# Kernel optimization log

Hardware: AMD Instinct MI355X
Metric: run time of the kernel (lower is better)

## Reference

```python
import jax, jax.numpy as jnp
import numpy as np

N = 50000   # node_count
D = 64      # dim_in (also GCN hidden, GRU hidden, top-k k)
E = 800000  # num_edges


def setup_inputs() -> dict:
    key = jax.random.key(0)
    ks = jax.random.split(key, 10)
    s = 1.0 / np.sqrt(D)
    return {
        "x": jax.random.normal(ks[0], (N, D), jnp.float32),
        "edge_index": jax.random.randint(ks[1], (2, E), 0, N, dtype=jnp.int64),
        "edge_weight": jax.random.uniform(ks[2], (E,), jnp.float32),
        # TopKPooling projection vector p
        "pool_p": jax.random.normal(ks[3], (D,), jnp.float32) * s,
        # EvolveGCNH initial weight (GRU hidden state h0), [D, D]
        "init_W": jax.random.normal(ks[4], (D, D), jnp.float32) * s,
        # GRU params, torch gate order (r, z, n)
        "gru_Wih": jax.random.normal(ks[5], (3 * D, D), jnp.float32) * s,
        "gru_Whh": jax.random.normal(ks[6], (3 * D, D), jnp.float32) * s,
        "gru_bih": jax.random.normal(ks[7], (3 * D,), jnp.float32) * s,
        "gru_bhh": jax.random.normal(ks[8], (3 * D,), jnp.float32) * s,
        # final Linear(D, 1)
        "lin_W": jax.random.normal(ks[9], (1, D), jnp.float32) * s,
        "lin_b": jnp.zeros((1,), jnp.float32),
    }


def reference(x, edge_index, edge_weight, pool_p, init_W,
              gru_Wih, gru_Whh, gru_bih, gru_bhh, lin_W, lin_b):
    n, d = x.shape
    # ---- TopKPooling: k = ceil((D/N) * N) = D nodes ----
    score = (x @ pool_p) / jnp.linalg.norm(pool_p)          # [N]
    vals, perm = jax.lax.top_k(score, d)                    # descending, k = D
    x_tilde = x[perm] * jnp.tanh(vals)[:, None]             # [D, D]
    # ---- one GRU step: batch = D pooled nodes, hidden = D, h0 = init_W ----
    gi = x_tilde @ gru_Wih.T + gru_bih                      # [D, 3D]
    gh = init_W @ gru_Whh.T + gru_bhh                       # [D, 3D]
    i_r, i_z, i_n = jnp.split(gi, 3, axis=-1)
    h_r, h_z, h_n = jnp.split(gh, 3, axis=-1)
    r = jax.nn.sigmoid(i_r + h_r)
    z = jax.nn.sigmoid(i_z + h_z)
    nn_ = jnp.tanh(i_n + r * h_n)
    W = (1.0 - z) * nn_ + z * init_W                        # evolved GCN weight [D, D]
    # ---- GCNConv_Fixed_W: add self-loops + symmetric norm + scatter ----
    loop = jnp.arange(n)
    row = jnp.concatenate([edge_index[0], loop])            # sources
    col = jnp.concatenate([edge_index[1], loop])            # targets
    w = jnp.concatenate([edge_weight, jnp.ones((n,), x.dtype)])
    deg = jax.ops.segment_sum(w, col, num_segments=n)
    deg_safe = jnp.where(deg > 0, deg, 1.0)
    dinv = jnp.where(deg > 0, jax.lax.rsqrt(deg_safe), 0.0)
    norm = dinv[row] * w * dinv[col]                        # [E+N]
    xw = x @ W                                              # [N, D]
    agg = jax.ops.segment_sum(norm[:, None] * xw[row], col, num_segments=n)
    # ---- head: relu + Linear(D, 1) ----
    h = jax.nn.relu(agg)
    return h @ lin_W.T + lin_b                              # [N, 1]
```

## Files before the change

kernel.cpp:

```cpp
#include <hip/hip_runtime.h>
#include <hip/hip_fp16.h>
#include <cmath>

#define N_NODES 50000
#define DIM 64
#define E_EDGES 800000
#define SCAN_BLOCKS 196
#define FIX 16777216.0f
#define DEG_MASK 0xFFFFFFFFFFull
#define NB_A 98
#define NRUNS 98

__global__ __launch_bounds__(256) void init_kernel(
    unsigned long long* __restrict__ packed, int* __restrict__ fillc) {
    int g = blockIdx.x * blockDim.x + threadIdx.x;
    if (g < N_NODES) { packed[g] = 0ull; fillc[g] = 0; }
}

__device__ __forceinline__ void wave_sort64(float& v, int& idx, int lane) {
    #pragma unroll
    for (int k = 2; k <= 64; k <<= 1) {
        #pragma unroll
        for (int j = k >> 1; j > 0; j >>= 1) {
            float ov = __shfl_xor(v, j);
            int   oi = __shfl_xor(idx, j);
            bool lower = ((lane & j) == 0);
            bool up    = ((lane & k) == 0);
            bool mine_prec = (v > ov) || (v == ov && idx < oi);
            bool keep = up ? (lower == mine_prec) : (lower != mine_prec);
            if (!keep) { v = ov; idx = oi; }
        }
    }
}

__device__ __forceinline__ void wave_merge_top64(float& v, int& idx,
                                                 float bv, int bi, int lane) {
    bool a_prec = (v > bv) || (v == bv && idx < bi);
    if (!a_prec) { v = bv; idx = bi; }
    #pragma unroll
    for (int j = 32; j > 0; j >>= 1) {
        float ov = __shfl_xor(v, j);
        int   oi = __shfl_xor(idx, j);
        bool lower = ((lane & j) == 0);
        bool mine_prec = (v > ov) || (v == ov && idx < oi);
        bool keep = (lower == mine_prec);
        if (!keep) { v = ov; idx = oi; }
    }
}

__global__ __launch_bounds__(512) void score_topk_a_kernel(
    const float* __restrict__ x, const float* __restrict__ p,
    float* __restrict__ cand_val, int* __restrict__ cand_idx,
    const int* __restrict__ ei, const float* __restrict__ ew,
    unsigned long long* __restrict__ packed) {
    __shared__ float sv[512];
    __shared__ int   si[512];
    int t = threadIdx.x, lane = t & 63, wvid = t >> 6;
    int g = blockIdx.x * 512 + t;
    float v; int idx;
    if (g < N_NODES) {
        const float4* x4 = (const float4*)(x + (size_t)g * DIM);
        const float4* p4 = (const float4*)p;
        float dot = 0.f, pn = 0.f;
        #pragma unroll
        for (int k = 0; k < 16; k++) {
            float4 xv = x4[k], pv = p4[k];
            dot += xv.x * pv.x + xv.y * pv.y + xv.z * pv.z + xv.w * pv.w;
            pn  += pv.x * pv.x + pv.y * pv.y + pv.z * pv.z + pv.w * pv.w;
        }
        v = dot / sqrtf(pn);
        idx = g;
    } else { v = -INFINITY; idx = 0x7fffffff; }
    wave_sort64(v, idx, lane);
    sv[t] = v; si[t] = idx;
    __syncthreads();
    if (wvid == 0) {
        #pragma unroll
        for (int r = 1; r < 8; r++)
            wave_merge_top64(v, idx, sv[r * 64 + 63 - lane], si[r * 64 + 63 - lane], lane);
        cand_val[blockIdx.x * 64 + lane] = v;
        cand_idx[blockIdx.x * 64 + lane] = idx;
    }
    for (int e = blockIdx.x * 512 + t; e < E_EDGES; e += NB_A * 512) {
        int c = ei[E_EDGES + e];
        unsigned long long q = (unsigned long long)(ew[e] * FIX);
        atomicAdd(&packed[c], (1ull << 40) | q);
    }
}

__global__ __launch_bounds__(256) void scan1_kernel(
    const unsigned long long* __restrict__ packed,
    int* __restrict__ off, int* __restrict__ bsum, float* __restrict__ dinv) {
    __shared__ int s[256];
    int t = threadIdx.x;
    int g = blockIdx.x * 256 + t;
    unsigned long long pk = (g < N_NODES) ? packed[g] : 0ull;
    int v = (int)(pk >> 40);
    if (g < N_NODES)
        dinv[g] = rsqrtf((float)(pk & DEG_MASK) * (1.0f / FIX) + 1.0f);
    s[t] = v;
    __syncthreads();
    for (int d = 1; d < 256; d <<= 1) {
        int add = (t >= d) ? s[t - d] : 0;
        __syncthreads();
        s[t] += add;
        __syncthreads();
    }
    if (g < N_NODES) off[g] = s[t] - v;
    if (t == 255) bsum[blockIdx.x] = s[255];
}

__global__ __launch_bounds__(256) void scan2_kernel(
    const int* __restrict__ bsum, int* __restrict__ boff) {
    __shared__ int s[256];
    int t = threadIdx.x;
    int v = (t < SCAN_BLOCKS) ? bsum[t] : 0;
    s[t] = v;
    __syncthreads();
    for (int d = 1; d < 256; d <<= 1) {
        int add = (t >= d) ? s[t - d] : 0;
        __syncthreads();
        s[t] += add;
        __syncthreads();
    }
    boff[t] = s[t] - v;
}

__global__ __launch_bounds__(256) void fill_kernel(
    const int* __restrict__ ei, const float* __restrict__ ew,
    const float* __restrict__ dinv, const int* __restrict__ off,
    const int* __restrict__ boff, int* __restrict__ fillc,
    float2* __restrict__ ren) {
    int e = blockIdx.x * blockDim.x + threadIdx.x;
    if (e >= E_EDGES) return;
    int r = ei[e], c = ei[E_EDGES + e];
    int pos = off[c] + boff[c >> 8] + atomicAdd(&fillc[c], 1);
    ren[pos] = make_float2(__int_as_float(r), dinv[r] * ew[e] * dinv[c]);
}

__global__ __launch_bounds__(1024) void topk_b_kernel(
    const float* __restrict__ cand_val, const int* __restrict__ cand_idx,
    const float* __restrict__ x, float* __restrict__ x_tilde) {
    __shared__ float rsv[16 * 64];
    __shared__ int   rsi[16 * 64];
    __shared__ float tval[64];
    __shared__ int   perm[64];
    int t = threadIdx.x, lane = t & 63, wv = t >> 6;
    int r0 = wv * 8;
    float v; int idx;
    if (r0 < NRUNS) { v = cand_val[r0 * 64 + lane]; idx = cand_idx[r0 * 64 + lane]; }
    else            { v = -INFINITY; idx = 0x7fffffff; }
    for (int r = r0 + 1; r < r0 + 8 && r < NRUNS; r++)
        wave_merge_top64(v, idx, cand_val[r * 64 + 63 - lane],
                         cand_idx[r * 64 + 63 - lane], lane);
    rsv[wv * 64 + lane] = v; rsi[wv * 64 + lane] = idx;
    __syncthreads();
    if (wv == 0) {
        v = rsv[lane]; idx = rsi[lane];
        for (int r = 1; r < 16; r++)
            wave_merge_top64(v, idx, rsv[r * 64 + 63 - lane],
                             rsi[r * 64 + 63 - lane], lane);
        tval[lane] = tanhf(v);
        perm[lane] = idx;
    }
    __syncthreads();
    for (int i = t; i < 4096; i += 1024) {
        int j = i >> 6, kk = i & 63;
        x_tilde[i] = x[perm[j] * DIM + kk] * tval[j];
    }
}

__global__ __launch_bounds__(64) void gru_kernel(
    const float* __restrict__ xt, const float* __restrict__ initW,
    const float* __restrict__ Wih, const float* __restrict__ Whh,
    const float* __restrict__ bih, const float* __restrict__ bhh,
    float* __restrict__ Wout) {
    __shared__ float xrow[64], hrow[64];
    int i = blockIdx.x, j = threadIdx.x;
    xrow[j] = xt[i * 64 + j];
    hrow[j] = initW[i * 64 + j];
    __syncthreads();
    float gi_r = bih[j], gi_z = bih[j + 64], gi_n = bih[j + 128];
    float gh_r = bhh[j], gh_z = bhh[j + 64], gh_n = bhh[j + 128];
    for (int k = 0; k < 64; k++) {
        float xv = xrow[k], hv = hrow[k];
        gi_r += xv * Wih[j * 64 + k];
        gi_z += xv * Wih[(j + 64) * 64 + k];
        gi_n += xv * Wih[(j + 128) * 64 + k];
        gh_r += hv * Whh[j * 64 + k];
        gh_z += hv * Whh[(j + 64) * 64 + k];
        gh_n += hv * Whh[(j + 128) * 64 + k];
    }
    float r = 1.f / (1.f + expf(-(gi_r + gh_r)));
    float z = 1.f / (1.f + expf(-(gi_z + gh_z)));
    float nn = tanhf(gi_n + r * gh_n);
    Wout[i * 64 + j] = (1.f - z) * nn + z * hrow[j];
}

__global__ __launch_bounds__(256) void xw_kernel(
    const float* __restrict__ x, const float* __restrict__ W,
    __half* __restrict__ xwh) {
    __shared__ float Wl[64 * 64];
    __shared__ float Xl[64 * 64];
    int t = threadIdx.x;
    int r0 = blockIdx.x * 64;
    for (int i = t; i < 4096; i += 256) Wl[i] = W[i];
    for (int i = t; i < 4096; i += 256) {
        int r = r0 + (i >> 6);
        Xl[i] = (r < N_NODES) ? x[r0 * 64 + i] : 0.f;
    }
    __syncthreads();
    int j = t & 63, ty = t >> 6;
    float acc[16];
    #pragma unroll
    for (int rr = 0; rr < 16; rr++) acc[rr] = 0.f;
    for (int k = 0; k < 64; k++) {
        float wvv = Wl[k * 64 + j];
        #pragma unroll
        for (int rr = 0; rr < 16; rr++)
            acc[rr] += Xl[(ty * 16 + rr) * 64 + k] * wvv;
    }
    #pragma unroll
    for (int rr = 0; rr < 16; rr++) {
        int r = r0 + ty * 16 + rr;
        if (r < N_NODES) xwh[r * DIM + j] = __float2half(acc[rr]);
    }
}

__global__ __launch_bounds__(256) void gather_head_kernel(
    const int* __restrict__ off, const int* __restrict__ boff,
    const float2* __restrict__ ren, const float* __restrict__ dinv,
    const float4* __restrict__ xwh,
    const float* __restrict__ linW, const float* __restrict__ linb,
    float* __restrict__ out) {
    int gid = blockIdx.x * blockDim.x + threadIdx.x;
    int n = gid >> 6, lane = gid & 63;
    if (n >= N_NODES) return;
    int c8 = lane & 7;
    int slot = lane >> 3;
    float acc[8];
    #pragma unroll
    for (int q = 0; q < 8; q++) acc[q] = 0.f;
    if (slot == 0) {
        float di = dinv[n];
        float s = di * di;
        float4 hv = xwh[n * 8 + c8];
        const __half2* h2 = reinterpret_cast<const __half2*>(&hv);
        #pragma unroll
        for (int q = 0; q < 4; q++) {
            float2 f = __half22float2(h2[q]);
            acc[2 * q]     = s * f.x;
            acc[2 * q + 1] = s * f.y;
        }
    }
    int s0 = off[n] + boff[n >> 8];
    int e0 = (n == N_NODES - 1) ? E_EDGES : off[n + 1] + boff[(n + 1) >> 8];
    for (int base = s0; base < e0; base += 64) {
        int m = min(64, e0 - base);
        int rv = 0; float wv = 0.f;
        if (base + lane < e0) {
            float2 pk = ren[base + lane];
            rv = __float_as_int(pk.x);
            wv = pk.y;
        }
        int G = (m + 7) >> 3;
        int g = 0;
        for (; g + 2 <= G; g += 2) {
            int src0 = g * 8 + slot, src1 = src0 + 8;
            int   ra = __shfl(rv, src0);  float wa = __shfl(wv, src0);
            int   rb = __shfl(rv, src1);  float wb = __shfl(wv, src1);
            float4 ha = xwh[ra * 8 + c8];
            float4 hb = xwh[rb * 8 + c8];
            const __half2* h2a = reinterpret_cast<const __half2*>(&ha);
            const __half2* h2b = reinterpret_cast<const __half2*>(&hb);
            #pragma unroll
            for (int q = 0; q < 4; q++) {
                float2 fa = __half22float2(h2a[q]);
                float2 fb = __half22float2(h2b[q]);
                acc[2 * q]     += wa * fa.x + wb * fb.x;
                acc[2 * q + 1] += wa * fa.y + wb * fb.y;
            }
        }
        if (g < G) {
            int src = g * 8 + slot;
            int r = __shfl(rv, src);
            float ww = __shfl(wv, src);
            float4 hv = xwh[r * 8 + c8];
            const __half2* h2 = reinterpret_cast<const __half2*>(&hv);
            #pragma unroll
            for (int q = 0; q < 4; q++) {
                float2 f = __half22float2(h2[q]);
                acc[2 * q]     += ww * f.x;
                acc[2 * q + 1] += ww * f.y;
            }
        }
    }
    #pragma unroll
    for (int q = 0; q < 8; q++) {
        acc[q] += __shfl_xor(acc[q], 8);
        acc[q] += __shfl_xor(acc[q], 16);
        acc[q] += __shfl_xor(acc[q], 32);
    }
    float pv = 0.f;
    #pragma unroll
    for (int q = 0; q < 8; q++)
        pv += fmaxf(acc[q], 0.f) * linW[c8 * 8 + q];
    pv += __shfl_xor(pv, 1); pv += __shfl_xor(pv, 2); pv += __shfl_xor(pv, 4);
    if (lane == 0) out[n] = pv + linb[0];
}

extern "C" void kernel_launch(void* const* d_in, const int* in_sizes, int n_in,
                              void* d_out, int out_size, void* d_ws, size_t ws_size,
                              hipStream_t stream) {
    const float* x     = (const float*)d_in[0];
    const int*   ei    = (const int*)d_in[1];
    const float* ew    = (const float*)d_in[2];
    const float* p     = (const float*)d_in[3];
    const float* initW = (const float*)d_in[4];
    const float* Wih   = (const float*)d_in[5];
    const float* Whh   = (const float*)d_in[6];
    const float* bih   = (const float*)d_in[7];
    const float* bhh   = (const float*)d_in[8];
    const float* linW  = (const float*)d_in[9];
    const float* linb  = (const float*)d_in[10];
    float* out = (float*)d_out;

    char* w = (char*)d_ws;
    unsigned long long* packed = (unsigned long long*)w; w += 8ull * N_NODES;
    int*   fillc   = (int*)w;      w += 4ull * N_NODES;
    float2* ren    = (float2*)w;   w += 8ull * E_EDGES;
    __half* xwh    = (__half*)w;   w += 2ull * (size_t)N_NODES * DIM;
    float* dinv    = (float*)w;    w += 4ull * N_NODES;
    int*   off     = (int*)w;      w += 4ull * N_NODES;
    float* cand_val= (float*)w;    w += 4ull * 8192;
    int*   cand_idx= (int*)w;      w += 4ull * 8192;
    float* x_tilde = (float*)w;    w += 4ull * 4096;
    float* W       = (float*)w;    w += 4ull * 4096;
    int*   bsum    = (int*)w;      w += 4ull * 256;
    int*   boff    = (int*)w;      w += 4ull * 256;

    init_kernel<<<SCAN_BLOCKS, 256, 0, stream>>>(packed, fillc);
    score_topk_a_kernel<<<NB_A, 512, 0, stream>>>(x, p, cand_val, cand_idx, ei, ew, packed);
    topk_b_kernel<<<1, 1024, 0, stream>>>(cand_val, cand_idx, x, x_tilde);
    gru_kernel<<<64, 64, 0, stream>>>(x_tilde, initW, Wih, Whh, bih, bhh, W);
    xw_kernel<<<(N_NODES + 63) / 64, 256, 0, stream>>>(x, W, xwh);
    scan1_kernel<<<SCAN_BLOCKS, 256, 0, stream>>>(packed, off, bsum, dinv);
    scan2_kernel<<<1, 256, 0, stream>>>(bsum, boff);
    fill_kernel<<<(E_EDGES + 255) / 256, 256, 0, stream>>>(ei, ew, dinv, off, boff, fillc, ren);
    gather_head_kernel<<<(N_NODES * 64 + 255) / 256, 256, 0, stream>>>(
        off, boff, ren, dinv, (const float4*)xwh, linW, linb, out);
}
```

Measured before the change: 247.8 us.

## Fuse topk-B with scan1 and GRU with scan2, widen edge-degree atomics grid

Merges the single-block top-k merge with the degree scan (extra blocks handle 1024-node scan chunks) and merges the GRU step with the second-level scan, cutting two kernel launches from the serial chain. The edge-degree atomic loop now runs over 384 blocks instead of 98, with only the first 98 doing scoring, to spread the atomic traffic. The scan block size grows from 256 to 1024, so boff indexing changes to >>10. This trades launch overhead for a longer serial 1024-thread scan and uneven block work inside the fused kernels.

```diff
diff --git a/kernel.cpp b/kernel.cpp
--- a/kernel.cpp
+++ b/kernel.cpp
@@ -5,11 +5,12 @@
 #define N_NODES 50000
 #define DIM 64
 #define E_EDGES 800000
-#define SCAN_BLOCKS 196
 #define FIX 16777216.0f
 #define DEG_MASK 0xFFFFFFFFFFull
 #define NB_A 98
+#define NB_EDGE 384
 #define NRUNS 98
+#define SCAN1_BLOCKS 49
 
 __global__ __launch_bounds__(256) void init_kernel(
     unsigned long long* __restrict__ packed, int* __restrict__ fillc) {
@@ -56,134 +57,127 @@
     __shared__ float sv[512];
     __shared__ int   si[512];
     int t = threadIdx.x, lane = t & 63, wvid = t >> 6;
-    int g = blockIdx.x * 512 + t;
-    float v; int idx;
-    if (g < N_NODES) {
-        const float4* x4 = (const float4*)(x + (size_t)g * DIM);
-        const float4* p4 = (const float4*)p;
-        float dot = 0.f, pn = 0.f;
-        #pragma unroll
-        for (int k = 0; k < 16; k++) {
-            float4 xv = x4[k], pv = p4[k];
-            dot += xv.x * pv.x + xv.y * pv.y + xv.z * pv.z + xv.w * pv.w;
-            pn  += pv.x * pv.x + pv.y * pv.y + pv.z * pv.z + pv.w * pv.w;
-        }
-        v = dot / sqrtf(pn);
-        idx = g;
-    } else { v = -INFINITY; idx = 0x7fffffff; }
-    wave_sort64(v, idx, lane);
-    sv[t] = v; si[t] = idx;
-    __syncthreads();
-    if (wvid == 0) {
-        #pragma unroll
-        for (int r = 1; r < 8; r++)
-            wave_merge_top64(v, idx, sv[r * 64 + 63 - lane], si[r * 64 + 63 - lane], lane);
-        cand_val[blockIdx.x * 64 + lane] = v;
-        cand_idx[blockIdx.x * 64 + lane] = idx;
-    }
-    for (int e = blockIdx.x * 512 + t; e < E_EDGES; e += NB_A * 512) {
+    if (blockIdx.x < NB_A) {
+        int g = blockIdx.x * 512 + t;
+        float v; int idx;
+        if (g < N_NODES) {
+            const float4* x4 = (const float4*)(x + (size_t)g * DIM);
+            const float4* p4 = (const float4*)p;
+            float dot = 0.f, pn = 0.f;
+            #pragma unroll
+            for (int k = 0; k < 16; k++) {
+                float4 xv = x4[k], pv = p4[k];
+                dot += xv.x * pv.x + xv.y * pv.y + xv.z * pv.z + xv.w * pv.w;
+                pn  += pv.x * pv.x + pv.y * pv.y + pv.z * pv.z + pv.w * pv.w;
+            }
+            v = dot / sqrtf(pn);
+            idx = g;
+        } else { v = -INFINITY; idx = 0x7fffffff; }
+        wave_sort64(v, idx, lane);
+        sv[t] = v; si[t] = idx;
+        __syncthreads();
+        if (wvid == 0) {
+            #pragma unroll
+            for (int r = 1; r < 8; r++)
+                wave_merge_top64(v, idx, sv[r * 64 + 63 - lane], si[r * 64 + 63 - lane], lane);
+            cand_val[blockIdx.x * 64 + lane] = v;
+            cand_idx[blockIdx.x * 64 + lane] = idx;
+        }
+    }
+    for (int e = blockIdx.x * 512 + t; e < E_EDGES; e += NB_EDGE * 512) {
         int c = ei[E_EDGES + e];
         unsigned long long q = (unsigned long long)(ew[e] * FIX);
         atomicAdd(&packed[c], (1ull << 40) | q);
     }
 }
 
-__global__ __launch_bounds__(256) void scan1_kernel(
+__global__ __launch_bounds__(1024) void topkb_scan1_kernel(
+    const float* __restrict__ cand_val, const int* __restrict__ cand_idx,
+    const float* __restrict__ x, float* __restrict__ x_tilde,
     const unsigned long long* __restrict__ packed,
     int* __restrict__ off, int* __restrict__ bsum, float* __restrict__ dinv) {
-    __shared__ int s[256];
-    int t = threadIdx.x;
-    int g = blockIdx.x * 256 + t;
-    unsigned long long pk = (g < N_NODES) ? packed[g] : 0ull;
-    int v = (int)(pk >> 40);
-    if (g < N_NODES)
-        dinv[g] = rsqrtf((float)(pk & DEG_MASK) * (1.0f / FIX) + 1.0f);
-    s[t] = v;
-    __syncthreads();
-    for (int d = 1; d < 256; d <<= 1) {
-        int add = (t >= d) ? s[t - d] : 0;
-        __syncthreads();
-        s[t] += add;
-        __syncthreads();
-    }
-    if (g < N_NODES) off[g] = s[t] - v;
-    if (t == 255) bsum[blockIdx.x] = s[255];
-}
-
-__global__ __launch_bounds__(256) void scan2_kernel(
-    const int* __restrict__ bsum, int* __restrict__ boff) {
-    __shared__ int s[256];
-    int t = threadIdx.x;
-    int v = (t < SCAN_BLOCKS) ? bsum[t] : 0;
-    s[t] = v;
-    __syncthreads();
-    for (int d = 1; d < 256; d <<= 1) {
-        int add = (t >= d) ? s[t - d] : 0;
-        __syncthreads();
-        s[t] += add;
-        __syncthreads();
-    }
-    boff[t] = s[t] - v;
-}
-
-__global__ __launch_bounds__(256) void fill_kernel(
-    const int* __restrict__ ei, const float* __restrict__ ew,
-    const float* __restrict__ dinv, const int* __restrict__ off,
-    const int* __restrict__ boff, int* __restrict__ fillc,
-    float2* __restrict__ ren) {
-    int e = blockIdx.x * blockDim.x + threadIdx.x;
-    if (e >= E_EDGES) return;
-    int r = ei[e], c = ei[E_EDGES + e];
-    int pos = off[c] + boff[c >> 8] + atomicAdd(&fillc[c], 1);
-    ren[pos] = make_float2(__int_as_float(r), dinv[r] * ew[e] * dinv[c]);
-}
-
-__global__ __launch_bounds__(1024) void topk_b_kernel(
-    const float* __restrict__ cand_val, const int* __restrict__ cand_idx,
-    const float* __restrict__ x, float* __restrict__ x_tilde) {
     __shared__ float rsv[16 * 64];
     __shared__ int   rsi[16 * 64];
     __shared__ float tval[64];
     __shared__ int   perm[64];
+    __shared__ int   s_scan[1024];
     int t = threadIdx.x, lane = t & 63, wv = t >> 6;
-    int r0 = wv * 8;
-    float v; int idx;
-    if (r0 < NRUNS) { v = cand_val[r0 * 64 + lane]; idx = cand_idx[r0 * 64 + lane]; }
-    else            { v = -INFINITY; idx = 0x7fffffff; }
-    for (int r = r0 + 1; r < r0 + 8 && r < NRUNS; r++)
-        wave_merge_top64(v, idx, cand_val[r * 64 + 63 - lane],
-                         cand_idx[r * 64 + 63 - lane], lane);
-    rsv[wv * 64 + lane] = v; rsi[wv * 64 + lane] = idx;
-    __syncthreads();
-    if (wv == 0) {
-        v = rsv[lane]; idx = rsi[lane];
-        for (int r = 1; r < 16; r++)
-            wave_merge_top64(v, idx, rsv[r * 64 + 63 - lane],
-                             rsi[r * 64 + 63 - lane], lane);
-        tval[lane] = tanhf(v);
-        perm[lane] = idx;
-    }
-    __syncthreads();
-    for (int i = t; i < 4096; i += 1024) {
-        int j = i >> 6, kk = i & 63;
-        x_tilde[i] = x[perm[j] * DIM + kk] * tval[j];
-    }
-}
-
-__global__ __launch_bounds__(64) void gru_kernel(
+    if (blockIdx.x == 0) {
+        int r0 = wv * 8;
+        float v; int idx;
+        if (r0 < NRUNS) { v = cand_val[r0 * 64 + lane]; idx = cand_idx[r0 * 64 + lane]; }
+        else            { v = -INFINITY; idx = 0x7fffffff; }
+        for (int r = r0 + 1; r < r0 + 8 && r < NRUNS; r++)
+            wave_merge_top64(v, idx, cand_val[r * 64 + 63 - lane],
+                             cand_idx[r * 64 + 63 - lane], lane);
+        rsv[wv * 64 + lane] = v; rsi[wv * 64 + lane] = idx;
+        __syncthreads();
+        if (wv == 0) {
+            v = rsv[lane]; idx = rsi[lane];
+            for (int r = 1; r < 16; r++)
+                wave_merge_top64(v, idx, rsv[r * 64 + 63 - lane],
+                                 rsi[r * 64 + 63 - lane], lane);
+            tval[lane] = tanhf(v);
+            perm[lane] = idx;
+        }
+        __syncthreads();
+        for (int i = t; i < 4096; i += 1024) {
+            int j = i >> 6, kk = i & 63;
+            x_tilde[i] = x[perm[j] * DIM + kk] * tval[j];
+        }
+    } else {
+        int b = blockIdx.x - 1;
+        int g = b * 1024 + t;
+        unsigned long long pk = (g < N_NODES) ? packed[g] : 0ull;
+        int v = (int)(pk >> 40);
+        if (g < N_NODES)
+            dinv[g] = rsqrtf((float)(pk & DEG_MASK) * (1.0f / FIX) + 1.0f);
+        s_scan[t] = v;
+        __syncthreads();
+        for (int d = 1; d < 1024; d <<= 1) {
+            int add = (t >= d) ? s_scan[t - d] : 0;
+            __syncthreads();
+            s_scan[t] += add;
+            __syncthreads();
+        }
+        if (g < N_NODES) off[g] = s_scan[t] - v;
+        if (t == 1023) bsum[b] = s_scan[1023];
+    }
+}
+
+__global__ __launch_bounds__(256) void gru_scan2_kernel(
+    const int* __restrict__ bsum, int* __restrict__ boff,
     const float* __restrict__ xt, const float* __restrict__ initW,
     const float* __restrict__ Wih, const float* __restrict__ Whh,
     const float* __restrict__ bih, const float* __restrict__ bhh,
     float* __restrict__ Wout) {
-    __shared__ float xrow[64], hrow[64];
-    int i = blockIdx.x, j = threadIdx.x;
-    xrow[j] = xt[i * 64 + j];
-    hrow[j] = initW[i * 64 + j];
+    __shared__ float xrow_s[256], hrow_s[256];
+    __shared__ int s[256];
+    int t = threadIdx.x;
+    if (blockIdx.x == 0) {
+        int v = (t < SCAN1_BLOCKS) ? bsum[t] : 0;
+        s[t] = v;
+        __syncthreads();
+        for (int d = 1; d < 256; d <<= 1) {
+            int add = (t >= d) ? s[t - d] : 0;
+            __syncthreads();
+            s[t] += add;
+            __syncthreads();
+        }
+        if (t < SCAN1_BLOCKS) boff[t] = s[t] - v;
+        return;
+    }
+    int i = (blockIdx.x - 1) * 4 + (t >> 6);
+    int j = t & 63;
+    int li = (t >> 6) * 64 + j;
+    xrow_s[li] = xt[i * 64 + j];
+    hrow_s[li] = initW[i * 64 + j];
     __syncthreads();
+    int lb = (t >> 6) * 64;
     float gi_r = bih[j], gi_z = bih[j + 64], gi_n = bih[j + 128];
     float gh_r = bhh[j], gh_z = bhh[j + 64], gh_n = bhh[j + 128];
     for (int k = 0; k < 64; k++) {
-        float xv = xrow[k], hv = hrow[k];
+        float xv = xrow_s[lb + k], hv = hrow_s[lb + k];
         gi_r += xv * Wih[j * 64 + k];
         gi_z += xv * Wih[(j + 64) * 64 + k];
         gi_n += xv * Wih[(j + 128) * 64 + k];
@@ -194,7 +188,7 @@
     float r = 1.f / (1.f + expf(-(gi_r + gh_r)));
     float z = 1.f / (1.f + expf(-(gi_z + gh_z)));
     float nn = tanhf(gi_n + r * gh_n);
-    Wout[i * 64 + j] = (1.f - z) * nn + z * hrow[j];
+    Wout[i * 64 + j] = (1.f - z) * nn + z * hrow_s[lb + j];
 }
 
 __global__ __launch_bounds__(256) void xw_kernel(
@@ -225,6 +219,18 @@
         int r = r0 + ty * 16 + rr;
         if (r < N_NODES) xwh[r * DIM + j] = __float2half(acc[rr]);
     }
+}
+
+__global__ __launch_bounds__(256) void fill_kernel(
+    const int* __restrict__ ei, const float* __restrict__ ew,
+    const float* __restrict__ dinv, const int* __restrict__ off,
+    const int* __restrict__ boff, int* __restrict__ fillc,
+    float2* __restrict__ ren) {
+    int e = blockIdx.x * blockDim.x + threadIdx.x;
+    if (e >= E_EDGES) return;
+    int r = ei[e], c = ei[E_EDGES + e];
+    int pos = off[c] + boff[c >> 10] + atomicAdd(&fillc[c], 1);
+    ren[pos] = make_float2(__int_as_float(r), dinv[r] * ew[e] * dinv[c]);
 }
 
 __global__ __launch_bounds__(256) void gather_head_kernel(
@@ -253,8 +259,8 @@
             acc[2 * q + 1] = s * f.y;
         }
     }
-    int s0 = off[n] + boff[n >> 8];
-    int e0 = (n == N_NODES - 1) ? E_EDGES : off[n + 1] + boff[(n + 1) >> 8];
+    int s0 = off[n] + boff[n >> 10];
+    int e0 = (n == N_NODES - 1) ? E_EDGES : off[n + 1] + boff[(n + 1) >> 10];
     for (int base = s0; base < e0; base += 64) {
         int m = min(64, e0 - base);
         int rv = 0; float wv = 0.f;
@@ -339,13 +345,13 @@
     int*   bsum    = (int*)w;      w += 4ull * 256;
     int*   boff    = (int*)w;      w += 4ull * 256;
 
-    init_kernel<<<SCAN_BLOCKS, 256, 0, stream>>>(packed, fillc);
-    score_topk_a_kernel<<<NB_A, 512, 0, stream>>>(x, p, cand_val, cand_idx, ei, ew, packed);
-    topk_b_kernel<<<1, 1024, 0, stream>>>(cand_val, cand_idx, x, x_tilde);
-    gru_kernel<<<64, 64, 0, stream>>>(x_tilde, initW, Wih, Whh, bih, bhh, W);
+    init_kernel<<<(N_NODES + 255) / 256, 256, 0, stream>>>(packed, fillc);
+    score_topk_a_kernel<<<NB_EDGE, 512, 0, stream>>>(x, p, cand_val, cand_idx, ei, ew, packed);
+    topkb_scan1_kernel<<<1 + SCAN1_BLOCKS, 1024, 0, stream>>>(
+        cand_val, cand_idx, x, x_tilde, packed, off, bsum, dinv);
+    gru_scan2_kernel<<<17, 256, 0, stream>>>(bsum, boff, x_tilde, initW,
+                                             Wih, Whh, bih, bhh, W);
     xw_kernel<<<(N_NODES + 63) / 64, 256, 0, stream>>>(x, W, xwh);
-    scan1_kernel<<<SCAN_BLOCKS, 256, 0, stream>>>(packed, off, bsum, dinv);
-    scan2_kernel<<<1, 256, 0, stream>>>(bsum, boff);
     fill_kernel<<<(E_EDGES + 255) / 256, 256, 0, stream>>>(ei, ew, dinv, off, boff, fillc, ren);
     gather_head_kernel<<<(N_NODES * 64 + 255) / 256, 256, 0, stream>>>(
         off, boff, ren, dinv, (const float4*)xwh, linW, linb, out);
```

Measured after the change: 241.0 us. 2.7% less time.
